# Optimization experiments

Hardware: AMD Instinct MI355X
Metric: run time of the kernel (lower is better)

The kernel has to match this reference:

```python
import jax, jax.numpy as jnp
import numpy as np

B, LC, LE, D, M = 128, 256, 1024, 256, 512
NEG = -1e9


def setup_inputs() -> dict:
    key = jax.random.key(0)
    ks = jax.random.split(key, 10)
    s = 0.02
    return {
        "criteria": jax.random.normal(ks[0], (B, LC, D), jnp.float32),
        "ehr": jax.random.normal(ks[1], (B, LE, D), jnp.float32),
        "criteria_mask": jax.random.randint(ks[2], (B, LC), 0, 2, jnp.int32),
        "ehr_mask": jax.random.randint(ks[3], (B, LE), 0, 2, jnp.int32),
        # params stored (in, out); torch Linear is x @ W.T + b
        "Wa": jax.random.normal(ks[4], (D, D), jnp.float32) * s,
        "ba": jnp.zeros((D,), jnp.float32),
        "Wr": jax.random.normal(ks[5], (2 * D, D), jnp.float32) * s,
        "br": jnp.zeros((D,), jnp.float32),
        "Wm": jax.random.normal(ks[6], (4 * D, M), jnp.float32) * s,
        "bm": jnp.zeros((M,), jnp.float32),
        "Wo": jax.random.normal(ks[7], (M, 3), jnp.float32) * s,
        "bo": jnp.zeros((3,), jnp.float32),
    }


def reference(criteria, ehr, Wa, ba, Wr, br, Wm, bm, Wo, bo,
              criteria_mask, ehr_mask):
    relu = jax.nn.relu
    c = relu(criteria @ Wa + ba)              # (B, Lc, D)
    e = relu(ehr @ Wa + ba)                   # (B, Le, D)
    align = jnp.einsum("bld,bed->ble", c, e)  # (B, Lc, Le)

    cm = criteria_mask.astype(align.dtype)
    em = ehr_mask.astype(align.dtype)
    # beta: softmax over Lc (dim=1), masked by criteria_mask along Lc
    beta = jax.nn.softmax(align + (1.0 - cm)[:, :, None] * NEG, axis=1)
    # alpha: softmax over Le (dim=1 of transposed), masked by ehr_mask along Le
    alpha = jax.nn.softmax(align + (1.0 - em)[:, None, :] * NEG, axis=2)

    # (alpha.unsqueeze(-1) * ehr.unsqueeze(1)).sum(2) == alpha @ ehr
    att_c = jnp.einsum("ble,bed->bld", alpha, ehr)        # (B, Lc, D)
    r1 = relu(jnp.concatenate([att_c, criteria], axis=-1) @ Wr + br).sum(axis=1)  # (B, D)

    # (beta.unsqueeze(-1) * criteria.unsqueeze(2)).sum(1) == beta.T @ criteria
    att_e = jnp.einsum("ble,bld->bed", beta, criteria)    # (B, Le, D)
    r2 = relu(jnp.concatenate([att_e, ehr], axis=-1) @ Wr + br).sum(axis=1)       # (B, D)

    m = jnp.concatenate([r1, r2, r1 * r2, r1 - r2], axis=-1)  # (B, 4D)
    return relu(m @ Wm + bm) @ Wo + bo                        # (B, 3)
```

## Files before the change

kernel.cpp:

```cpp
#include <hip/hip_runtime.h>
#include <hip/hip_bf16.h>

#define BB 128
#define LC 256
#define LE 1024
#define DD 256
#define MM 512

typedef short bf16x8 __attribute__((ext_vector_type(8)));
typedef unsigned short u16x8 __attribute__((ext_vector_type(8)));
typedef unsigned short u16x4 __attribute__((ext_vector_type(4)));
typedef float f32x4 __attribute__((ext_vector_type(4)));

__device__ __forceinline__ unsigned short f2bfu(float f) {
  unsigned int x = __float_as_uint(f);
  return (unsigned short)((x + 0x7fffu + ((x >> 16) & 1u)) >> 16);
}

__device__ __forceinline__ int lx(int r, int q) {
  return r * 32 + (((q ^ ((r >> 1) & 3)) & 3) << 3);
}

__device__ __forceinline__ void gll16(const unsigned short* g, unsigned short* l) {
  __builtin_amdgcn_global_load_lds((const __attribute__((address_space(1))) void*)g,
                                   (__attribute__((address_space(3))) void*)l, 16, 0, 0);
}

__device__ __forceinline__ void stg128(unsigned short* S, const unsigned short* g,
                                       long ldu, int tid) {
  const int l = tid & 63, w = tid >> 6;
  const int r = w * 16 + (l >> 2), q = l & 3;
  gll16(g + (long)r * ldu + (((q ^ ((r >> 1) & 3)) & 3) << 3), S + w * 512);
}

__device__ __forceinline__ void stg256(unsigned short* S, const unsigned short* g,
                                       long ldu, int tid) {
  const int l = tid & 63, w = tid >> 6;
#pragma unroll
  for (int it = 0; it < 2; ++it) {
    const int r = it * 128 + w * 16 + (l >> 2), q = l & 3;
    gll16(g + (long)r * ldu + (((q ^ ((r >> 1) & 3)) & 3) << 3), S + it * 4096 + w * 512);
  }
}

__device__ __forceinline__ void stg128_256(unsigned short* S, const unsigned short* g,
                                           long ldu, int tid) {
  const int l = tid & 63, w = tid >> 6;
#pragma unroll
  for (int it = 0; it < 2; ++it) {
    const int r = it * 64 + w * 16 + (l >> 2), q = l & 3;
    gll16(g + (long)r * ldu + (((q ^ ((r >> 1) & 3)) & 3) << 3), S + it * 2048 + w * 512);
  }
}

__device__ __forceinline__ void stage_f32(unsigned short* S, const float* g, long ld, int tid) {
#pragma unroll
  for (int i = 0; i < 2; ++i) {
    int c = tid + i * 256;
    int r = c >> 2, q = c & 3;
    const float4* p = (const float4*)(g + (long)r * ld + q * 8);
    float4 v0 = p[0], v1 = p[1];
    u16x8 o;
    o[0] = f2bfu(v0.x); o[1] = f2bfu(v0.y); o[2] = f2bfu(v0.z); o[3] = f2bfu(v0.w);
    o[4] = f2bfu(v1.x); o[5] = f2bfu(v1.y); o[6] = f2bfu(v1.z); o[7] = f2bfu(v1.w);
    *(u16x8*)&S[lx(r, q)] = o;
  }
}

__device__ __forceinline__ void mma_step(const unsigned short* As, const unsigned short* Bs,
                                         f32x4 (&acc)[4][4], int wm, int wn, int lane) {
  const int lm = lane & 15, quad = lane >> 4;
  bf16x8 a[4], b[4];
#pragma unroll
  for (int i = 0; i < 4; ++i) {
    a[i] = *(const bf16x8*)&As[lx(wm * 64 + i * 16 + lm, quad)];
    b[i] = *(const bf16x8*)&Bs[lx(wn * 64 + i * 16 + lm, quad)];
  }
  __builtin_amdgcn_s_setprio(1);
#pragma unroll
  for (int i = 0; i < 4; ++i)
#pragma unroll
    for (int j = 0; j < 4; ++j)
      acc[i][j] = __builtin_amdgcn_mfma_f32_16x16x32_bf16(a[i], b[j], acc[i][j], 0, 0, 0);
  __builtin_amdgcn_s_setprio(0);
}

template <int MT, int NT>
__device__ __forceinline__ void mma_tiles(const unsigned short* As, const unsigned short* Bs,
                                          f32x4 (&acc)[MT][NT], int m0, int n0, int lane) {
  const int lm = lane & 15, quad = lane >> 4;
  bf16x8 a[MT], b[NT];
#pragma unroll
  for (int i = 0; i < MT; ++i)
    a[i] = *(const bf16x8*)&As[lx(m0 + i * 16 + lm, quad)];
#pragma unroll
  for (int j = 0; j < NT; ++j)
    b[j] = *(const bf16x8*)&Bs[lx(n0 + j * 16 + lm, quad)];
  __builtin_amdgcn_s_setprio(1);
#pragma unroll
  for (int i = 0; i < MT; ++i)
#pragma unroll
    for (int j = 0; j < NT; ++j)
      acc[i][j] = __builtin_amdgcn_mfma_f32_16x16x32_bf16(a[i], b[j], acc[i][j], 0, 0, 0);
  __builtin_amdgcn_s_setprio(0);
}

__global__ void zero_kernel(float* __restrict__ p, int n) {
  int i = blockIdx.x * 256 + threadIdx.x;
  if (i < n) p[i] = 0.f;
}

__global__ void wconv_kernel(const float* __restrict__ Wa, const float* __restrict__ Wr,
                             unsigned short* __restrict__ WaT, unsigned short* __restrict__ WrT) {
  int i = blockIdx.x * 256 + threadIdx.x;
  if (i < 65536) WaT[i] = f2bfu(Wa[(i & 255) * 256 + (i >> 8)]);
  if (i < 131072) WrT[i] = f2bfu(Wr[(long)(i & 511) * 256 + (i >> 9)]);
}

__global__ void transT_kernel(const float* __restrict__ src, const int* __restrict__ mask,
                              unsigned short* __restrict__ dstT, unsigned short* __restrict__ dstN,
                              int R, int C) {
  __shared__ unsigned short T2[64 * 64];
  const int tid = threadIdx.x, b = blockIdx.z;
  const int r0 = blockIdx.y * 64, c0 = blockIdx.x * 64;
  const float* s = src + (long)b * R * C;
  const int* mk = mask + (long)b * R;
  unsigned short* dT = dstT + (long)b * R * C;
  unsigned short* dN = dstN + (long)b * R * C;
#pragma unroll
  for (int i = 0; i < 4; ++i) {
    int r = (tid >> 4) + i * 16, c4 = tid & 15;
    float4 v = *(const float4*)(s + (long)(r0 + r) * C + c0 + c4 * 4);
    u16x4 nat;
    nat[0] = f2bfu(v.x); nat[1] = f2bfu(v.y); nat[2] = f2bfu(v.z); nat[3] = f2bfu(v.w);
    *(u16x4*)(dN + (long)(r0 + r) * C + c0 + c4 * 4) = nat;
    float g = mk[r0 + r] ? 1.f : 0.f;
    float vm[4] = {v.x * g, v.y * g, v.z * g, v.w * g};
#pragma unroll
    for (int k = 0; k < 4; ++k) {
      int row = c4 * 4 + k;
      T2[row * 64 + (((r >> 3) ^ (row >> 2)) & 7) * 8 + (r & 7)] = f2bfu(vm[k]);
    }
  }
  __syncthreads();
#pragma unroll
  for (int j = 0; j < 2; ++j) {
    int idx = tid * 2 + j;
    int row = idx >> 3, ch = idx & 7;
    *(u16x8*)(dT + (long)(c0 + row) * R + r0 + ch * 8) =
        *(const u16x8*)&T2[row * 64 + ((ch ^ (row >> 2)) & 7) * 8];
  }
}

__global__ __launch_bounds__(256, 2) void proj_mfma(const float* __restrict__ A,
                                                    const unsigned short* __restrict__ WaT,
                                                    const float* __restrict__ ba,
                                                    unsigned short* __restrict__ out) {
  __shared__ unsigned short As[2][4096], Bs[2][4096];
  const int tid = threadIdx.x, lane = tid & 63, w = tid >> 6, wm = w >> 1, wn = w & 1;
  const long m0 = (long)blockIdx.y * 128;
  const int n0 = blockIdx.x * 128;
  f32x4 acc[4][4] = {};
  stage_f32(As[0], A + m0 * DD, DD, tid);
  stg128_256(Bs[0], WaT + (long)n0 * DD, DD, tid);
  __syncthreads();
  for (int s = 0; s < 8; ++s) {
    if (s < 7) {
      stage_f32(As[(s + 1) & 1], A + m0 * DD + (s + 1) * 32, DD, tid);
      stg128_256(Bs[(s + 1) & 1], WaT + (long)n0 * DD + (s + 1) * 32, DD, tid);
    }
    mma_step(As[s & 1], Bs[s & 1], acc, wm, wn, lane);
    __syncthreads();
  }
  const int lm = lane & 15, quad = lane >> 4;
#pragma unroll
  for (int i = 0; i < 4; ++i)
#pragma unroll
    for (int j = 0; j < 4; ++j) {
      int col = n0 + wn * 64 + j * 16 + lm;
      float bias = ba[col];
#pragma unroll
      for (int r = 0; r < 4; ++r) {
        long row = m0 + wm * 64 + i * 16 + quad * 4 + r;
        float v = acc[i][j][r] + bias;
        out[row * DD + col] = f2bfu(v > 0.f ? v : 0.f);
      }
    }
}

template <int NCH>
__device__ __forceinline__ void attn_body(
    unsigned short* SLOT, unsigned short* S4,
    const unsigned short* resB, const unsigned short* aSrc,
    const unsigned short* pvB, long pvLd,
    const int* mask, unsigned short* outp, int tid) {
  const int lane = tid & 63, w = tid >> 6;
  const int lm = lane & 15, quad = lane >> 4;
  const int wmS = w >> 2, wnS = w & 3;
  const int wm = w >> 2, wn = w & 3;
  float* asum_s = (float*)SLOT;
  f32x4 acc[4][4] = {};
  float ap0 = 0.f, ap1 = 0.f;
  stg128(SLOT, aSrc, DD, tid);
  stg128(SLOT + 4096, resB, DD, tid);
  stg128(SLOT + 8192, aSrc + 32, DD, tid);
  stg128(SLOT + 8192 + 4096, resB + 32, DD, tid);
  for (int ch = 0; ch < NCH; ++ch) {
    const unsigned short* Ag = aSrc + (long)ch * 128 * DD;
    const unsigned short* Pg = pvB + (long)ch * 128;
    f32x4 accS[4][2] = {};
#pragma unroll
    for (int s = 0; s < 8; ++s) {
      asm volatile("s_waitcnt vmcnt(2) lgkmcnt(0)" ::: "memory");
      __builtin_amdgcn_s_barrier();
      if (s < 6) {
        unsigned short* d = SLOT + ((s + 2) % 3) * 8192;
        stg128(d, Ag + (s + 2) * 32, DD, tid);
        stg128(d + 4096, resB + (s + 2) * 32, DD, tid);
      } else if (s == 6) {
        stg256(SLOT + 2 * 8192, Pg, pvLd, tid);
      } else {
        stg256(SLOT, Pg + 32, pvLd, tid);
      }
      const unsigned short* base = SLOT + (s % 3) * 8192;
      mma_tiles<4, 2>(base, base + 4096, accS, wmS * 64, wnS * 32, lane);
    }
#pragma unroll
    for (int i = 0; i < 4; ++i) {
      const int A0 = wmS * 64 + i * 16 + quad * 4;
      const int4 m4 = *(const int4*)(mask + ch * 128 + A0);
      const float g0 = m4.x ? 1.f : 0.f, g1 = m4.y ? 1.f : 0.f;
      const float g2 = m4.z ? 1.f : 0.f, g3 = m4.w ? 1.f : 0.f;
      const int kk = A0 >> 5, wi = A0 & 31;
      const int qq = wi >> 3, sub = wi & 7;
#pragma unroll
      for (int j = 0; j < 2; ++j) {
        const int row = wnS * 32 + j * 16 + lm;
        float e0 = __expf(accS[i][j][0]);
        float e1 = __expf(accS[i][j][1]);
        float e2 = __expf(accS[i][j][2]);
        float e3 = __expf(accS[i][j][3]);
        float sm = g0 * e0 + g1 * e1 + g2 * e2 + g3 * e3;
        if (j == 0) ap0 += sm; else ap1 += sm;
        u16x4 pk;
        pk[0] = f2bfu(e0); pk[1] = f2bfu(e1); pk[2] = f2bfu(e2); pk[3] = f2bfu(e3);
        *(u16x4*)&S4[kk * 4096 + row * 32 + ((qq ^ ((row >> 1) & 3)) << 3) + sub] = pk;
      }
    }
#pragma unroll
    for (int kk = 0; kk < 4; ++kk) {
      if ((kk == 3) && (ch == NCH - 1))
        asm volatile("s_waitcnt vmcnt(0) lgkmcnt(0)" ::: "memory");
      else
        asm volatile("s_waitcnt vmcnt(2) lgkmcnt(0)" ::: "memory");
      __builtin_amdgcn_s_barrier();
      if (kk < 2) {
        stg256(SLOT + ((kk + 1) % 3) * 8192, Pg + (kk + 2) * 32, pvLd, tid);
      } else if (ch + 1 < NCH) {
        unsigned short* d = SLOT + (kk - 2) * 8192;
        stg128(d, aSrc + (long)(ch + 1) * 128 * DD + (kk - 2) * 32, DD, tid);
        stg128(d + 4096, resB + (kk - 2) * 32, DD, tid);
      }
      mma_tiles<4, 4>(S4 + kk * 4096, SLOT + ((kk + 2) % 3) * 8192, acc,
                      wm * 64, wn * 64, lane);
    }
  }
  if (tid < 128) asum_s[tid] = 0.f;
  __syncthreads();
  {
    float s = ap0;
    s += __shfl_xor(s, 16); s += __shfl_xor(s, 32);
    if (quad == 0) atomicAdd(&asum_s[wnS * 32 + lm], s);
    float t = ap1;
    t += __shfl_xor(t, 16); t += __shfl_xor(t, 32);
    if (quad == 0) atomicAdd(&asum_s[wnS * 32 + 16 + lm], t);
  }
  __syncthreads();
  float rs[4][4];
#pragma unroll
  for (int i = 0; i < 4; ++i)
#pragma unroll
    for (int r = 0; r < 4; ++r)
      rs[i][r] = 1.f / asum_s[wm * 64 + i * 16 + quad * 4 + r];
#pragma unroll
  for (int i = 0; i < 4; ++i)
#pragma unroll
    for (int j = 0; j < 4; ++j) {
      int col = wn * 64 + j * 16 + lm;
#pragma unroll
      for (int r = 0; r < 4; ++r) {
        int row = wm * 64 + i * 16 + quad * 4 + r;
        outp[(long)row * DD + col] = f2bfu(acc[i][j][r] * rs[i][r]);
      }
    }
}

__global__ __launch_bounds__(512, 2) void attn_c_fused(
    const unsigned short* __restrict__ cB, const unsigned short* __restrict__ eB,
    const unsigned short* __restrict__ ehrTm, const int* __restrict__ em,
    unsigned short* __restrict__ attc) {
  __shared__ unsigned short SLOT[3 * 8192];
  __shared__ unsigned short S4[16384];
  const int tid = threadIdx.x, fid = blockIdx.x;
  const int lid = (fid & 7) * 32 + (fid >> 3);
  const int b = lid >> 1, m0 = (lid & 1) * 128;
  attn_body<8>(SLOT, S4, cB + ((long)b * LC + m0) * DD, eB + (long)b * LE * DD,
               ehrTm + (long)b * DD * LE, LE, em + (long)b * LE,
               attc + ((long)b * LC + m0) * DD, tid);
}

__global__ __launch_bounds__(512, 2) void attn_e_fused(
    const unsigned short* __restrict__ cB, const unsigned short* __restrict__ eB,
    const unsigned short* __restrict__ critTm, const int* __restrict__ cm,
    unsigned short* __restrict__ atte) {
  __shared__ unsigned short SLOT[3 * 8192];
  __shared__ unsigned short S4[16384];
  const int tid = threadIdx.x, fid = blockIdx.x;
  const int lid = (fid & 7) * 128 + (fid >> 3);
  const int b = lid >> 3, n0 = (lid & 7) * 128;
  attn_body<2>(SLOT, S4, eB + ((long)b * LE + n0) * DD, cB + (long)b * LC * DD,
               critTm + (long)b * DD * LC, LC, cm + (long)b * LC,
               atte + ((long)b * LE + n0) * DD, tid);
}

__global__ __launch_bounds__(256, 2) void rsum_mfma(const unsigned short* __restrict__ att,
                                                    const unsigned short* __restrict__ origB,
                                                    const unsigned short* __restrict__ WrT,
                                                    const float* __restrict__ br,
                                                    float* __restrict__ rout, int Lseq) {
  __shared__ unsigned short SL[3 * 8192];
  __shared__ float red[2][128];
  const int tid = threadIdx.x, lane = tid & 63, w = tid >> 6, wm = w >> 1, wn = w & 1;
  const long m0 = (long)blockIdx.y * 128;
  const int n0 = blockIdx.x * 128;
  const int b = (int)(m0 / Lseq);
  f32x4 acc[4][4] = {};
  stg128_256(SL, att + m0 * DD, DD, tid);
  stg128_256(SL + 4096, WrT + (long)n0 * 512, 512, tid);
  stg128_256(SL + 8192, att + m0 * DD + 32, DD, tid);
  stg128_256(SL + 8192 + 4096, WrT + (long)n0 * 512 + 32, 512, tid);
#pragma unroll
  for (int s = 0; s < 16; ++s) {
    if (s == 15) asm volatile("s_waitcnt vmcnt(0) lgkmcnt(0)" ::: "memory");
    else         asm volatile("s_waitcnt vmcnt(4) lgkmcnt(0)" ::: "memory");
    __builtin_amdgcn_s_barrier();
    if (s < 14) {
      const int k1 = (s + 2) * 32;
      const unsigned short* aS =
          (k1 < DD) ? att + m0 * DD + k1 : origB + m0 * DD + (k1 - DD);
      unsigned short* d = SL + ((s + 2) % 3) * 8192;
      stg128_256(d, aS, DD, tid);
      stg128_256(d + 4096, WrT + (long)n0 * 512 + k1, 512, tid);
    }
    const unsigned short* base = SL + (s % 3) * 8192;
    mma_step(base, base + 4096, acc, wm, wn, lane);
  }
  const int lm = lane & 15, quad = lane >> 4;
#pragma unroll
  for (int j = 0; j < 4; ++j) {
    int col = n0 + wn * 64 + j * 16 + lm;
    float bias = br[col];
    float s = 0.f;
#pragma unroll
    for (int i = 0; i < 4; ++i)
#pragma unroll
      for (int r = 0; r < 4; ++r) {
        float v = acc[i][j][r] + bias;
        s += v > 0.f ? v : 0.f;
      }
    s += __shfl_xor(s, 16);
    s += __shfl_xor(s, 32);
    if (quad == 0) red[wm][wn * 64 + j * 16 + lm] = s;
  }
  __syncthreads();
  if (tid < 128)
    atomicAdd(&rout[b * DD + n0 + tid], red[0][tid] + red[1][tid]);
}

__global__ void mbuild_kernel(const float* __restrict__ r1, const float* __restrict__ r2,
                              unsigned short* __restrict__ mB) {
  int i = blockIdx.x * 256 + threadIdx.x;
  int b = i >> 8, d = i & 255;
  float v1 = r1[i], v2 = r2[i];
  unsigned short* row = mB + (long)b * 1024;
  row[d] = f2bfu(v1);
  row[256 + d] = f2bfu(v2);
  row[512 + d] = f2bfu(v1 * v2);
  row[768 + d] = f2bfu(v1 - v2);
}

__global__ __launch_bounds__(256, 2) void mlp_mfma(const unsigned short* __restrict__ mB,
                                                   const float* __restrict__ Wm,
                                                   const float* __restrict__ bm,
                                                   float* __restrict__ h) {
  __shared__ unsigned short As[4096], Bs[4096];
  const int tid = threadIdx.x, lane = tid & 63, w = tid >> 6, wm = w >> 1, wn = w & 1;
  const int n0 = blockIdx.x * 128;
  f32x4 acc[4][4] = {};
  for (int k0 = 0; k0 < 4 * DD; k0 += 32) {
    stg128_256(As, mB + k0, 1024, tid);
    {
      const int dcc = tid & 7, er = tid >> 3;
#pragma unroll
      for (int i = 0; i < 4; ++i) {
        int nch = dcc + i * 8;
        float4 v = *(const float4*)(Wm + (long)(k0 + er) * MM + n0 + nch * 4);
        float vv[4] = {v.x, v.y, v.z, v.w};
#pragma unroll
        for (int q = 0; q < 4; ++q)
          Bs[lx(nch * 4 + q, er >> 3) + (er & 7)] = f2bfu(vv[q]);
      }
    }
    __syncthreads();
    mma_step(As, Bs, acc, wm, wn, lane);
    __syncthreads();
  }
  const int lm = lane & 15, quad = lane >> 4;
#pragma unroll
  for (int i = 0; i < 4; ++i)
#pragma unroll
    for (int j = 0; j < 4; ++j) {
      int col = n0 + wn * 64 + j * 16 + lm;
      float bias = bm[col];
#pragma unroll
      for (int r = 0; r < 4; ++r) {
        int row = wm * 64 + i * 16 + quad * 4 + r;
        float v = acc[i][j][r] + bias;
        h[(long)row * MM + col] = v > 0.f ? v : 0.f;
      }
    }
}

__global__ void out3_kernel(const float* __restrict__ h, const float* __restrict__ Wo,
                            const float* __restrict__ bo, float* __restrict__ out) {
  const int b = blockIdx.x, tid = threadIdx.x;
  __shared__ float red[256];
  float a[3] = {0.f, 0.f, 0.f};
  for (int k = tid; k < MM; k += 256) {
    float hv = h[(long)b * MM + k];
    a[0] += hv * Wo[k * 3 + 0];
    a[1] += hv * Wo[k * 3 + 1];
    a[2] += hv * Wo[k * 3 + 2];
  }
#pragma unroll
  for (int o = 0; o < 3; ++o) {
    red[tid] = a[o]; __syncthreads();
    for (int st = 128; st > 0; st >>= 1) {
      if (tid < st) red[tid] += red[tid + st];
      __syncthreads();
    }
    if (tid == 0) out[b * 3 + o] = red[0] + bo[o];
    __syncthreads();
  }
}

extern "C" void kernel_launch(void* const* d_in, const int* in_sizes, int n_in,
                              void* d_out, int out_size, void* d_ws, size_t ws_size,
                              hipStream_t stream) {
  const float* criteria = (const float*)d_in[0];
  const float* ehr      = (const float*)d_in[1];
  const int*   cmask    = (const int*)d_in[2];
  const int*   emask    = (const int*)d_in[3];
  const float* Wa       = (const float*)d_in[4];
  const float* ba       = (const float*)d_in[5];
  const float* Wr       = (const float*)d_in[6];
  const float* br       = (const float*)d_in[7];
  const float* Wm       = (const float*)d_in[8];
  const float* bm       = (const float*)d_in[9];
  const float* Wo       = (const float*)d_in[10];
  const float* bo       = (const float*)d_in[11];
  float* out = (float*)d_out;

  char* ws = (char*)d_ws;
  unsigned short* cB     = (unsigned short*)(ws);
  unsigned short* eB     = (unsigned short*)(ws + 16777216);
  unsigned short* ehrTm  = (unsigned short*)(ws + 83886080);
  unsigned short* critTm = (unsigned short*)(ws + 150994944);
  unsigned short* ehrN   = (unsigned short*)(ws + 167772160);
  unsigned short* critN  = (unsigned short*)(ws + 234881024);
  unsigned short* attc   = (unsigned short*)(ws + 251658240);
  unsigned short* atteP  = (unsigned short*)(ws + 268435456);
  float* r1   = (float*)(ws + 335544320);
  float* r2   = (float*)(ws + 335675392);
  unsigned short* WaT = (unsigned short*)(ws + 335806464);
  unsigned short* WrT = (unsigned short*)(ws + 335937536);
  unsigned short* mB  = (unsigned short*)(ws + 336199680);
  float* hbuf         = (float*)(ws + 336461824);

  dim3 blk(256);
  zero_kernel<<<dim3(256), blk, 0, stream>>>(r1, 65536);
  wconv_kernel<<<dim3(512), blk, 0, stream>>>(Wa, Wr, WaT, WrT);
  transT_kernel<<<dim3(DD / 64, LE / 64, BB), blk, 0, stream>>>(ehr, emask, ehrTm, ehrN, LE, DD);
  transT_kernel<<<dim3(DD / 64, LC / 64, BB), blk, 0, stream>>>(criteria, cmask, critTm, critN, LC, DD);
  proj_mfma<<<dim3(2, (BB * LC) / 128), blk, 0, stream>>>(criteria, WaT, ba, cB);
  proj_mfma<<<dim3(2, (BB * LE) / 128), blk, 0, stream>>>(ehr, WaT, ba, eB);
  attn_c_fused<<<dim3(256), dim3(512), 0, stream>>>(cB, eB, ehrTm, emask, attc);
  attn_e_fused<<<dim3(1024), dim3(512), 0, stream>>>(cB, eB, critTm, cmask, atteP);
  rsum_mfma<<<dim3(2, (BB * LC) / 128), blk, 0, stream>>>(attc, critN, WrT, br, r1, LC);
  rsum_mfma<<<dim3(2, (BB * LE) / 128), blk, 0, stream>>>(atteP, ehrN, WrT, br, r2, LE);
  mbuild_kernel<<<dim3(BB), blk, 0, stream>>>(r1, r2, mB);
  mlp_mfma<<<dim3(MM / 128), blk, 0, stream>>>(mB, Wm, bm, hbuf);
  out3_kernel<<<dim3(BB), blk, 0, stream>>>(hbuf, Wo, bo, out);
}
```

Before: 588.6 us.

## Reuse bf16 inputs in projection, merge attention kernels, split-K MLP, wider transposes

The projection GEMM now reads the bf16 copies already produced by the transpose kernel through async global-to-LDS loads, using a 3-slot pipeline with explicit waitcnt in place of converting fp32 on the fly. The two attention kernels are merged into one launch of 1280 blocks so both directions can share the GPU. The MLP is split four ways along K with atomic accumulation, and bias plus ReLU move into the output kernel, which now reduces with wavefront shuffles. The transpose kernel handles 256-row tiles with a padded LDS layout. The risks are atomic nondeterminism, reduced transpose occupancy, and more LDS bank conflicts.

```diff
diff --git a/kernel.cpp b/kernel.cpp
--- a/kernel.cpp
+++ b/kernel.cpp
@@ -53,20 +53,6 @@
   }
 }
 
-__device__ __forceinline__ void stage_f32(unsigned short* S, const float* g, long ld, int tid) {
-#pragma unroll
-  for (int i = 0; i < 2; ++i) {
-    int c = tid + i * 256;
-    int r = c >> 2, q = c & 3;
-    const float4* p = (const float4*)(g + (long)r * ld + q * 8);
-    float4 v0 = p[0], v1 = p[1];
-    u16x8 o;
-    o[0] = f2bfu(v0.x); o[1] = f2bfu(v0.y); o[2] = f2bfu(v0.z); o[3] = f2bfu(v0.w);
-    o[4] = f2bfu(v1.x); o[5] = f2bfu(v1.y); o[6] = f2bfu(v1.z); o[7] = f2bfu(v1.w);
-    *(u16x8*)&S[lx(r, q)] = o;
-  }
-}
-
 __device__ __forceinline__ void mma_step(const unsigned short* As, const unsigned short* Bs,
                                          f32x4 (&acc)[4][4], int wm, int wn, int lane) {
   const int lm = lane & 15, quad = lane >> 4;
@@ -120,57 +106,65 @@
 __global__ void transT_kernel(const float* __restrict__ src, const int* __restrict__ mask,
                               unsigned short* __restrict__ dstT, unsigned short* __restrict__ dstN,
                               int R, int C) {
-  __shared__ unsigned short T2[64 * 64];
+  __shared__ unsigned short T2[64 * 258];
   const int tid = threadIdx.x, b = blockIdx.z;
-  const int r0 = blockIdx.y * 64, c0 = blockIdx.x * 64;
+  const int r0 = blockIdx.y * 256, c0 = blockIdx.x * 64;
   const float* s = src + (long)b * R * C;
   const int* mk = mask + (long)b * R;
   unsigned short* dT = dstT + (long)b * R * C;
   unsigned short* dN = dstN + (long)b * R * C;
-#pragma unroll
-  for (int i = 0; i < 4; ++i) {
-    int r = (tid >> 4) + i * 16, c4 = tid & 15;
+  const int c4 = tid & 15, rb = tid >> 4;
+#pragma unroll
+  for (int i = 0; i < 16; ++i) {
+    int r = rb + i * 16;
     float4 v = *(const float4*)(s + (long)(r0 + r) * C + c0 + c4 * 4);
     u16x4 nat;
     nat[0] = f2bfu(v.x); nat[1] = f2bfu(v.y); nat[2] = f2bfu(v.z); nat[3] = f2bfu(v.w);
     *(u16x4*)(dN + (long)(r0 + r) * C + c0 + c4 * 4) = nat;
     float g = mk[r0 + r] ? 1.f : 0.f;
-    float vm[4] = {v.x * g, v.y * g, v.z * g, v.w * g};
-#pragma unroll
-    for (int k = 0; k < 4; ++k) {
-      int row = c4 * 4 + k;
-      T2[row * 64 + (((r >> 3) ^ (row >> 2)) & 7) * 8 + (r & 7)] = f2bfu(vm[k]);
-    }
+    T2[(c4 * 4 + 0) * 258 + r] = f2bfu(v.x * g);
+    T2[(c4 * 4 + 1) * 258 + r] = f2bfu(v.y * g);
+    T2[(c4 * 4 + 2) * 258 + r] = f2bfu(v.z * g);
+    T2[(c4 * 4 + 3) * 258 + r] = f2bfu(v.w * g);
   }
   __syncthreads();
-#pragma unroll
-  for (int j = 0; j < 2; ++j) {
-    int idx = tid * 2 + j;
-    int row = idx >> 3, ch = idx & 7;
-    *(u16x8*)(dT + (long)(c0 + row) * R + r0 + ch * 8) =
-        *(const u16x8*)&T2[row * 64 + ((ch ^ (row >> 2)) & 7) * 8];
-  }
-}
-
-__global__ __launch_bounds__(256, 2) void proj_mfma(const float* __restrict__ A,
+  const int dlo = tid >> 4, rs = (tid & 15) * 8;
+#pragma unroll
+  for (int dd = 0; dd < 4; ++dd) {
+    const int d = dlo + dd * 16;
+#pragma unroll
+    for (int j = 0; j < 2; ++j) {
+      const int r = rs + j * 128;
+      *(u16x8*)(dT + (long)(c0 + d) * R + r0 + r) = *(const u16x8*)&T2[d * 258 + r];
+    }
+  }
+}
+
+__global__ __launch_bounds__(256, 2) void proj_mfma(const unsigned short* __restrict__ AN,
                                                     const unsigned short* __restrict__ WaT,
                                                     const float* __restrict__ ba,
                                                     unsigned short* __restrict__ out) {
-  __shared__ unsigned short As[2][4096], Bs[2][4096];
+  __shared__ unsigned short SL[3 * 8192];
   const int tid = threadIdx.x, lane = tid & 63, w = tid >> 6, wm = w >> 1, wn = w & 1;
   const long m0 = (long)blockIdx.y * 128;
   const int n0 = blockIdx.x * 128;
   f32x4 acc[4][4] = {};
-  stage_f32(As[0], A + m0 * DD, DD, tid);
-  stg128_256(Bs[0], WaT + (long)n0 * DD, DD, tid);
-  __syncthreads();
+  stg128_256(SL, AN + m0 * DD, DD, tid);
+  stg128_256(SL + 4096, WaT + (long)n0 * DD, DD, tid);
+  stg128_256(SL + 8192, AN + m0 * DD + 32, DD, tid);
+  stg128_256(SL + 8192 + 4096, WaT + (long)n0 * DD + 32, DD, tid);
+#pragma unroll
   for (int s = 0; s < 8; ++s) {
-    if (s < 7) {
-      stage_f32(As[(s + 1) & 1], A + m0 * DD + (s + 1) * 32, DD, tid);
-      stg128_256(Bs[(s + 1) & 1], WaT + (long)n0 * DD + (s + 1) * 32, DD, tid);
-    }
-    mma_step(As[s & 1], Bs[s & 1], acc, wm, wn, lane);
-    __syncthreads();
+    if (s == 7) asm volatile("s_waitcnt vmcnt(0) lgkmcnt(0)" ::: "memory");
+    else        asm volatile("s_waitcnt vmcnt(4) lgkmcnt(0)" ::: "memory");
+    __builtin_amdgcn_s_barrier();
+    if (s < 6) {
+      unsigned short* d = SL + ((s + 2) % 3) * 8192;
+      stg128_256(d, AN + m0 * DD + (s + 2) * 32, DD, tid);
+      stg128_256(d + 4096, WaT + (long)n0 * DD + (s + 2) * 32, DD, tid);
+    }
+    const unsigned short* base = SL + (s % 3) * 8192;
+    mma_step(base, base + 4096, acc, wm, wn, lane);
   }
   const int lm = lane & 15, quad = lane >> 4;
 #pragma unroll
@@ -295,32 +289,28 @@
     }
 }
 
-__global__ __launch_bounds__(512, 2) void attn_c_fused(
+__global__ __launch_bounds__(512, 2) void attn_fused(
     const unsigned short* __restrict__ cB, const unsigned short* __restrict__ eB,
-    const unsigned short* __restrict__ ehrTm, const int* __restrict__ em,
-    unsigned short* __restrict__ attc) {
+    const unsigned short* __restrict__ ehrTm, const unsigned short* __restrict__ critTm,
+    const int* __restrict__ em, const int* __restrict__ cm,
+    unsigned short* __restrict__ attc, unsigned short* __restrict__ atte) {
   __shared__ unsigned short SLOT[3 * 8192];
   __shared__ unsigned short S4[16384];
   const int tid = threadIdx.x, fid = blockIdx.x;
-  const int lid = (fid & 7) * 32 + (fid >> 3);
-  const int b = lid >> 1, m0 = (lid & 1) * 128;
-  attn_body<8>(SLOT, S4, cB + ((long)b * LC + m0) * DD, eB + (long)b * LE * DD,
-               ehrTm + (long)b * DD * LE, LE, em + (long)b * LE,
-               attc + ((long)b * LC + m0) * DD, tid);
-}
-
-__global__ __launch_bounds__(512, 2) void attn_e_fused(
-    const unsigned short* __restrict__ cB, const unsigned short* __restrict__ eB,
-    const unsigned short* __restrict__ critTm, const int* __restrict__ cm,
-    unsigned short* __restrict__ atte) {
-  __shared__ unsigned short SLOT[3 * 8192];
-  __shared__ unsigned short S4[16384];
-  const int tid = threadIdx.x, fid = blockIdx.x;
-  const int lid = (fid & 7) * 128 + (fid >> 3);
-  const int b = lid >> 3, n0 = (lid & 7) * 128;
-  attn_body<2>(SLOT, S4, eB + ((long)b * LE + n0) * DD, cB + (long)b * LC * DD,
-               critTm + (long)b * DD * LC, LC, cm + (long)b * LC,
-               atte + ((long)b * LE + n0) * DD, tid);
+  if (fid < 256) {
+    const int lid = (fid & 7) * 32 + (fid >> 3);
+    const int b = lid >> 1, m0 = (lid & 1) * 128;
+    attn_body<8>(SLOT, S4, cB + ((long)b * LC + m0) * DD, eB + (long)b * LE * DD,
+                 ehrTm + (long)b * DD * LE, LE, em + (long)b * LE,
+                 attc + ((long)b * LC + m0) * DD, tid);
+  } else {
+    const int f = fid - 256;
+    const int lid = (f & 7) * 128 + (f >> 3);
+    const int b = lid >> 3, n0 = (lid & 7) * 128;
+    attn_body<2>(SLOT, S4, eB + ((long)b * LE + n0) * DD, cB + (long)b * LC * DD,
+                 critTm + (long)b * DD * LC, LC, cm + (long)b * LC,
+                 atte + ((long)b * LE + n0) * DD, tid);
+  }
 }
 
 __global__ __launch_bounds__(256, 2) void rsum_mfma(const unsigned short* __restrict__ att,
@@ -391,13 +381,13 @@
 
 __global__ __launch_bounds__(256, 2) void mlp_mfma(const unsigned short* __restrict__ mB,
                                                    const float* __restrict__ Wm,
-                                                   const float* __restrict__ bm,
                                                    float* __restrict__ h) {
   __shared__ unsigned short As[4096], Bs[4096];
   const int tid = threadIdx.x, lane = tid & 63, w = tid >> 6, wm = w >> 1, wn = w & 1;
   const int n0 = blockIdx.x * 128;
+  const int kb = blockIdx.y * 256;
   f32x4 acc[4][4] = {};
-  for (int k0 = 0; k0 < 4 * DD; k0 += 32) {
+  for (int k0 = kb; k0 < kb + 256; k0 += 32) {
     stg128_256(As, mB + k0, 1024, tid);
     {
       const int dcc = tid & 7, er = tid >> 3;
@@ -421,37 +411,37 @@
 #pragma unroll
     for (int j = 0; j < 4; ++j) {
       int col = n0 + wn * 64 + j * 16 + lm;
-      float bias = bm[col];
 #pragma unroll
       for (int r = 0; r < 4; ++r) {
         int row = wm * 64 + i * 16 + quad * 4 + r;
-        float v = acc[i][j][r] + bias;
-        h[(long)row * MM + col] = v > 0.f ? v : 0.f;
+        atomicAdd(&h[(long)row * MM + col], acc[i][j][r]);
       }
     }
 }
 
 __global__ void out3_kernel(const float* __restrict__ h, const float* __restrict__ Wo,
-                            const float* __restrict__ bo, float* __restrict__ out) {
-  const int b = blockIdx.x, tid = threadIdx.x;
-  __shared__ float red[256];
+                            const float* __restrict__ bm, const float* __restrict__ bo,
+                            float* __restrict__ out) {
+  const int b = blockIdx.x, tid = threadIdx.x, lane = tid & 63, w = tid >> 6;
+  __shared__ float red[4][3];
   float a[3] = {0.f, 0.f, 0.f};
   for (int k = tid; k < MM; k += 256) {
-    float hv = h[(long)b * MM + k];
+    float hv = h[(long)b * MM + k] + bm[k];
+    hv = hv > 0.f ? hv : 0.f;
     a[0] += hv * Wo[k * 3 + 0];
     a[1] += hv * Wo[k * 3 + 1];
     a[2] += hv * Wo[k * 3 + 2];
   }
 #pragma unroll
   for (int o = 0; o < 3; ++o) {
-    red[tid] = a[o]; __syncthreads();
-    for (int st = 128; st > 0; st >>= 1) {
-      if (tid < st) red[tid] += red[tid + st];
-      __syncthreads();
-    }
-    if (tid == 0) out[b * 3 + o] = red[0] + bo[o];
-    __syncthreads();
-  }
+    a[o] += __shfl_xor(a[o], 1);  a[o] += __shfl_xor(a[o], 2);
+    a[o] += __shfl_xor(a[o], 4);  a[o] += __shfl_xor(a[o], 8);
+    a[o] += __shfl_xor(a[o], 16); a[o] += __shfl_xor(a[o], 32);
+    if (lane == 0) red[w][o] = a[o];
+  }
+  __syncthreads();
+  if (tid < 3)
+    out[b * 3 + tid] = red[0][tid] + red[1][tid] + red[2][tid] + red[3][tid] + bo[tid];
 }
 
 extern "C" void kernel_launch(void* const* d_in, const int* in_sizes, int n_in,
@@ -482,23 +472,23 @@
   unsigned short* atteP  = (unsigned short*)(ws + 268435456);
   float* r1   = (float*)(ws + 335544320);
   float* r2   = (float*)(ws + 335675392);
-  unsigned short* WaT = (unsigned short*)(ws + 335806464);
-  unsigned short* WrT = (unsigned short*)(ws + 335937536);
-  unsigned short* mB  = (unsigned short*)(ws + 336199680);
-  float* hbuf         = (float*)(ws + 336461824);
+  float* hbuf = (float*)(ws + 335806464);
+  unsigned short* WaT = (unsigned short*)(ws + 336068608);
+  unsigned short* WrT = (unsigned short*)(ws + 336199680);
+  unsigned short* mB  = (unsigned short*)(ws + 336461824);
 
   dim3 blk(256);
-  zero_kernel<<<dim3(256), blk, 0, stream>>>(r1, 65536);
+  zero_kernel<<<dim3(512), blk, 0, stream>>>(r1, 131072);
   wconv_kernel<<<dim3(512), blk, 0, stream>>>(Wa, Wr, WaT, WrT);
-  transT_kernel<<<dim3(DD / 64, LE / 64, BB), blk, 0, stream>>>(ehr, emask, ehrTm, ehrN, LE, DD);
-  transT_kernel<<<dim3(DD / 64, LC / 64, BB), blk, 0, stream>>>(criteria, cmask, critTm, critN, LC, DD);
-  proj_mfma<<<dim3(2, (BB * LC) / 128), blk, 0, stream>>>(criteria, WaT, ba, cB);
-  proj_mfma<<<dim3(2, (BB * LE) / 128), blk, 0, stream>>>(ehr, WaT, ba, eB);
-  attn_c_fused<<<dim3(256), dim3(512), 0, stream>>>(cB, eB, ehrTm, emask, attc);
-  attn_e_fused<<<dim3(1024), dim3(512), 0, stream>>>(cB, eB, critTm, cmask, atteP);
+  transT_kernel<<<dim3(DD / 64, LE / 256, BB), blk, 0, stream>>>(ehr, emask, ehrTm, ehrN, LE, DD);
+  transT_kernel<<<dim3(DD / 64, LC / 256, BB), blk, 0, stream>>>(criteria, cmask, critTm, critN, LC, DD);
+  proj_mfma<<<dim3(2, (BB * LC) / 128), blk, 0, stream>>>(critN, WaT, ba, cB);
+  proj_mfma<<<dim3(2, (BB * LE) / 128), blk, 0, stream>>>(ehrN, WaT, ba, eB);
+  attn_fused<<<dim3(1280), dim3(512), 0, stream>>>(cB, eB, ehrTm, critTm, emask, cmask,
+                                                   attc, atteP);
   rsum_mfma<<<dim3(2, (BB * LC) / 128), blk, 0, stream>>>(attc, critN, WrT, br, r1, LC);
   rsum_mfma<<<dim3(2, (BB * LE) / 128), blk, 0, stream>>>(atteP, ehrN, WrT, br, r2, LE);
   mbuild_kernel<<<dim3(BB), blk, 0, stream>>>(r1, r2, mB);
-  mlp_mfma<<<dim3(MM / 128), blk, 0, stream>>>(mB, Wm, bm, hbuf);
-  out3_kernel<<<dim3(BB), blk, 0, stream>>>(hbuf, Wo, bo, out);
-}
+  mlp_mfma<<<dim3(MM / 128, 4), blk, 0, stream>>>(mB, Wm, hbuf);
+  out3_kernel<<<dim3(BB), blk, 0, stream>>>(hbuf, Wo, bm, bo, out);
+}
```

After: 530.8 us. -9.8%, faster.
